# Kernel optimization log

Hardware: AMD Instinct MI355X
Metric: run time of the kernel (lower is better)

Reference implementation:

```python
import jax, jax.numpy as jnp
import numpy as np

B, H, T, N = 8, 12, 1024, 256  # N = mlp_internal_dim_multiplier * n_embd // n_head = 4*768//12
THETA = 2.0 ** 16


def _rope(phases, v):
    # interleaved rotate-half: pairs (even, odd) -> (-odd, even), as in torch stack+view
    v_rot = jnp.stack((-v[..., 1::2], v[..., ::2]), axis=-1).reshape(v.shape)
    ang = (phases % 1.0) * (2.0 * jnp.pi)
    return v * jnp.cos(ang) + v_rot * jnp.sin(ang)


def setup_inputs() -> dict:
    key = jax.random.key(0)
    k1, k2 = jax.random.split(key)
    Q = jax.random.normal(k1, (B, H, T, N), dtype=jnp.float32)
    V = jax.random.normal(k2, (B, H, T, N), dtype=jnp.float32)
    # frozen RoPE frequency buffer: pairs share a frequency, theta=2**16 (cycles/position)
    idx = (jnp.arange(N) // 2 * 2).astype(jnp.float32)
    freqs = (THETA ** (-idx / N)).reshape(1, 1, 1, N)
    return {"Q": Q, "V": V, "freqs": freqs}


def reference(Q, V, freqs):
    t = Q.shape[2]
    pos = jnp.arange(t, dtype=freqs.dtype).reshape(1, 1, -1, 1)
    phases = pos * freqs                      # [1,1,T,N]
    QR = _rope(phases, Q)                     # K is Q in Vision-BDH, so KR = QR
    scale = 1.0 / jnp.sqrt(jnp.asarray(Q.shape[-1], Q.dtype))
    scores = jnp.einsum("bhtn,bhsn->bhts", QR, QR) * scale  # [B,H,T,T]
    attn = jax.nn.softmax(scores, axis=-1)
    return jnp.einsum("bhts,bhsn->bhtn", attn, V)
```

## Files before the change

kernel.cpp:

```cpp
#include <hip/hip_runtime.h>
#include <stdint.h>

typedef __attribute__((ext_vector_type(8))) short short8;
typedef __attribute__((ext_vector_type(4))) float f32x4;
typedef __attribute__((ext_vector_type(16))) float f32x16;

#define BH 96
#define T 1024
#define D 256

static __device__ __forceinline__ unsigned short f2bf(float x){
  uint32_t u = __float_as_uint(x);
  uint32_t r = (u + 0x7FFFu + ((u >> 16) & 1u)) >> 16;
  return (unsigned short)r;
}

static __device__ __forceinline__ uint32_t cvtpk_bf16(float lo, float hi){
  uint32_t r;
  asm("v_cvt_pk_bf16_f32 %0, %1, %2" : "=v"(r) : "v"(lo), "v"(hi));
  return r;
}

static __device__ __forceinline__ float exp2_fast(float x){
  float r;
  asm("v_exp_f32 %0, %1" : "=v"(r) : "v"(x));
  return r;
}

static __device__ __forceinline__ void gload_lds16(const void* g, void* l){
  __builtin_amdgcn_global_load_lds((const __attribute__((address_space(1))) void*)g,
                                   (__attribute__((address_space(3))) void*)l, 16, 0, 0);
}

__global__ void k_rope(const float* __restrict__ Q, const float* __restrict__ freqs,
                       unsigned short* __restrict__ QR){
  const float SC = 0.25f * 1.20112241f;
  long idx = (long)blockIdx.x * 256 + threadIdx.x;
  long e = idx * 4;
  int n = (int)(e & (D - 1));
  int t = (int)((e >> 8) & (T - 1));
  float4 q = *(const float4*)(Q + e);
  float f0 = freqs[n];
  float f2 = freqs[n + 2];
  float ph0 = (float)t * f0; ph0 -= floorf(ph0);
  float ph2 = (float)t * f2; ph2 -= floorf(ph2);
  float c0 = __builtin_amdgcn_cosf(ph0), s0 = __builtin_amdgcn_sinf(ph0);
  float c2 = __builtin_amdgcn_cosf(ph2), s2 = __builtin_amdgcn_sinf(ph2);
  float o0 = (q.x * c0 - q.y * s0) * SC;
  float o1 = (q.y * c0 + q.x * s0) * SC;
  float o2 = (q.z * c2 - q.w * s2) * SC;
  float o3 = (q.w * c2 + q.z * s2) * SC;
  ushort4 o;
  o.x = f2bf(o0); o.y = f2bf(o1); o.z = f2bf(o2); o.w = f2bf(o3);
  *(ushort4*)(QR + e) = o;
}

__global__ void k_transpose(const float* __restrict__ V, unsigned short* __restrict__ Vt){
  __shared__ unsigned short L[64 * 66];
  int bid = blockIdx.x;
  int head = bid >> 6;
  int rem = bid & 63;
  int t0 = (rem & 15) * 64;
  int n0 = (rem >> 4) * 64;
  int tid = threadIdx.x;
  const float* Vh = V + (long)head * T * D;
  unsigned short* Vth = Vt + (long)head * T * D;
  int lr = tid >> 4;
  int lc = (tid & 15) * 4;
#pragma unroll
  for (int i = 0; i < 4; ++i){
    int tl = i * 16 + lr;
    float4 v = *(const float4*)(Vh + (long)(t0 + tl) * D + n0 + lc);
    uint32_t w0 = (uint32_t)f2bf(v.x) | ((uint32_t)f2bf(v.y) << 16);
    uint32_t w1 = (uint32_t)f2bf(v.z) | ((uint32_t)f2bf(v.w) << 16);
    *(uint32_t*)&L[tl * 66 + lc]     = w0;
    *(uint32_t*)&L[tl * 66 + lc + 2] = w1;
  }
  __syncthreads();
  int nr = tid >> 3;
  int t8 = (tid & 7) * 8;
#pragma unroll
  for (int i = 0; i < 2; ++i){
    int n_row = i * 32 + nr;
    unsigned short u[8];
#pragma unroll
    for (int j = 0; j < 8; ++j) u[j] = L[(t8 + j) * 66 + n_row];
    uint4 o;
    o.x = (uint32_t)u[0] | ((uint32_t)u[1] << 16);
    o.y = (uint32_t)u[2] | ((uint32_t)u[3] << 16);
    o.z = (uint32_t)u[4] | ((uint32_t)u[5] << 16);
    o.w = (uint32_t)u[6] | ((uint32_t)u[7] << 16);
    *(uint4*)(Vth + (long)(n0 + n_row) * T + t0 + t8) = o;
  }
}

__global__ __launch_bounds__(256, 2) void k_flash(const unsigned short* __restrict__ QR,
                                                  const unsigned short* __restrict__ Vt,
                                                  float* __restrict__ Out){
  __shared__ short lds[2][16384];
  int tid = threadIdx.x;
  int wid = tid >> 6, lane = tid & 63;
  int q31 = lane & 31, h = lane >> 5;

  int b = blockIdx.x;
  int xx = b & 7, sw = b >> 3;
  int qt = sw & 7, hg = sw >> 3;
  int head = hg * 8 + xx;

  const unsigned short* qr = QR + (long)head * T * D;
  const unsigned short* vt = Vt + (long)head * T * D;
  int qb = qt * 128 + wid * 32;

  int bK[4], bV[4];
#pragma unroll
  for (int j = 0; j < 4; ++j){
    int i = tid + j * 256;
    int c = i >> 6, s = i & 63;
    bK[j] = (s & 31) * 256 + (s >> 5) * 8 + c * 16;
    bV[j] = ((c >> 1) * 32 + (s & 31)) * 1024 + (c & 1) * 16 + (s >> 5) * 8;
  }

  short8 qf[16];
#pragma unroll
  for (int c = 0; c < 16; ++c)
    qf[c] = *(const short8*)(qr + (long)(qb + q31) * D + c * 16 + h * 8);

  const f32x16 Zv = {0.f,0.f,0.f,0.f,0.f,0.f,0.f,0.f,0.f,0.f,0.f,0.f,0.f,0.f,0.f,0.f};
  f32x16 acc[8];
#pragma unroll
  for (int i = 0; i < 8; ++i) acc[i] = Zv;
  float m = -3e38f, lsum = 0.f;

#pragma unroll
  for (int j = 0; j < 4; ++j){
    int i = tid + j * 256;
    gload_lds16(qr + bK[j], &lds[0][i * 8]);
    gload_lds16(vt + bV[j], &lds[0][8192 + i * 8]);
  }
  asm volatile("s_waitcnt vmcnt(0)" ::: "memory");
  __syncthreads();

  int buf = 0;
  for (int kb = 0; kb < T; kb += 32){
    if (kb + 32 < T){
      const unsigned short* sk = qr + (long)(kb + 32) * 256;
      const unsigned short* sv = vt + (kb + 32);
#pragma unroll
      for (int j = 0; j < 4; ++j){
        int i = tid + j * 256;
        gload_lds16(sk + bK[j], &lds[buf ^ 1][i * 8]);
        gload_lds16(sv + bV[j], &lds[buf ^ 1][8192 + i * 8]);
      }
    }
    const short* ldsK = &lds[buf][0];
    const short* ldsV = &lds[buf][8192];

    f32x16 sA = Zv, sB = Zv;
    __builtin_amdgcn_s_setprio(1);
#pragma unroll
    for (int c = 0; c < 8; ++c){
      short8 kf = *(const short8*)&ldsK[c * 512 + lane * 8];
      sA = __builtin_amdgcn_mfma_f32_32x32x16_bf16(kf, qf[c], sA, 0, 0, 0);
    }
#pragma unroll
    for (int c = 8; c < 16; ++c){
      short8 kf = *(const short8*)&ldsK[c * 512 + lane * 8];
      sB = __builtin_amdgcn_mfma_f32_32x32x16_bf16(kf, qf[c], sB, 0, 0, 0);
    }
    __builtin_amdgcn_s_setprio(0);
    f32x16 sc = sA + sB;

    float lm = fmaxf(fmaxf(fmaxf(sc[0], sc[1]), fmaxf(sc[2], sc[3])),
                     fmaxf(fmaxf(sc[4], sc[5]), fmaxf(sc[6], sc[7])));
    lm = fmaxf(lm, fmaxf(fmaxf(fmaxf(sc[8], sc[9]), fmaxf(sc[10], sc[11])),
                         fmaxf(fmaxf(sc[12], sc[13]), fmaxf(sc[14], sc[15]))));
    lm = fmaxf(lm, __shfl_xor(lm, 32));
    if (__any(lm > m + 11.0f)){
      float mn = fmaxf(m, lm);
      float a = exp2_fast(m - mn);
      m = mn;
      lsum *= a;
#pragma unroll
      for (int nb = 0; nb < 8; ++nb) acc[nb] *= a;
    }
    f32x16 p;
#pragma unroll
    for (int e = 0; e < 16; ++e) p[e] = exp2_fast(sc[e] - m);
    lsum += (((p[0]+p[1])+(p[2]+p[3])) + ((p[4]+p[5])+(p[6]+p[7])))
          + (((p[8]+p[9])+(p[10]+p[11])) + ((p[12]+p[13])+(p[14]+p[15])));

    uint32_t X0 = cvtpk_bf16(p[0],  p[1]);
    uint32_t X1 = cvtpk_bf16(p[2],  p[3]);
    uint32_t Y0 = cvtpk_bf16(p[4],  p[5]);
    uint32_t Y1 = cvtpk_bf16(p[6],  p[7]);
    uint32_t sX0 = __shfl_xor(X0, 32), sX1 = __shfl_xor(X1, 32);
    uint32_t sY0 = __shfl_xor(Y0, 32), sY1 = __shfl_xor(Y1, 32);
    uint4 f0;
    f0.x = h ? sY0 : X0;
    f0.y = h ? sY1 : X1;
    f0.z = h ? Y0  : sX0;
    f0.w = h ? Y1  : sX1;
    uint32_t Z0 = cvtpk_bf16(p[8],  p[9]);
    uint32_t Z1 = cvtpk_bf16(p[10], p[11]);
    uint32_t W0 = cvtpk_bf16(p[12], p[13]);
    uint32_t W1 = cvtpk_bf16(p[14], p[15]);
    uint32_t sZ0 = __shfl_xor(Z0, 32), sZ1 = __shfl_xor(Z1, 32);
    uint32_t sW0 = __shfl_xor(W0, 32), sW1 = __shfl_xor(W1, 32);
    uint4 f1;
    f1.x = h ? sW0 : Z0;
    f1.y = h ? sW1 : Z1;
    f1.z = h ? W0  : sZ0;
    f1.w = h ? W1  : sZ1;
    short8 pF0 = __builtin_bit_cast(short8, f0);
    short8 pF1 = __builtin_bit_cast(short8, f1);

    __builtin_amdgcn_s_setprio(1);
#pragma unroll
    for (int nb = 0; nb < 8; ++nb){
      short8 v0 = *(const short8*)&ldsV[(nb * 2 + 0) * 512 + lane * 8];
      short8 v1 = *(const short8*)&ldsV[(nb * 2 + 1) * 512 + lane * 8];
      acc[nb] = __builtin_amdgcn_mfma_f32_32x32x16_bf16(v0, pF0, acc[nb], 0, 0, 0);
      acc[nb] = __builtin_amdgcn_mfma_f32_32x32x16_bf16(v1, pF1, acc[nb], 0, 0, 0);
    }
    __builtin_amdgcn_s_setprio(0);

    asm volatile("s_waitcnt vmcnt(0)" ::: "memory");
    __syncthreads();
    buf ^= 1;
  }

  lsum += __shfl_xor(lsum, 32);
  float r = 1.0f / lsum;
  float* op = Out + (long)head * T * D + (long)(qb + q31) * D + h * 4;
#pragma unroll
  for (int nb = 0; nb < 8; ++nb){
#pragma unroll
    for (int rq = 0; rq < 4; ++rq){
      f32x4 o;
      o.x = acc[nb][rq * 4 + 0] * r;
      o.y = acc[nb][rq * 4 + 1] * r;
      o.z = acc[nb][rq * 4 + 2] * r;
      o.w = acc[nb][rq * 4 + 3] * r;
      *(f32x4*)(op + nb * 32 + rq * 8) = o;
    }
  }
}

extern "C" void kernel_launch(void* const* d_in, const int* in_sizes, int n_in,
                              void* d_out, int out_size, void* d_ws, size_t ws_size,
                              hipStream_t stream){
  (void)in_sizes; (void)n_in; (void)out_size; (void)ws_size;
  const float* Q     = (const float*)d_in[0];
  const float* V     = (const float*)d_in[1];
  const float* freqs = (const float*)d_in[2];
  float* Out = (float*)d_out;
  unsigned short* QR = (unsigned short*)d_ws;
  unsigned short* Vt = QR + (size_t)BH * T * D;
  k_rope<<<dim3((BH * T * D) / 4 / 256), dim3(256), 0, stream>>>(Q, freqs, QR);
  k_transpose<<<dim3(BH * 64), dim3(256), 0, stream>>>(V, Vt);
  k_flash<<<dim3(BH * 8), dim3(256), 0, stream>>>(QR, Vt, Out);
}
```

Measured before the change: 218.2 us.

## Make flash kernel persistent with triple-buffered LDS and partial vmcnt waits

```diff
diff --git a/kernel.cpp b/kernel.cpp
--- a/kernel.cpp
+++ b/kernel.cpp
@@ -84,7 +84,7 @@
     int n_row = i * 32 + nr;
     unsigned short u[8];
 #pragma unroll
-    for (int j = 0; j < 8; ++j) u[j] = L[(t8 + j) * 66 + n_row];
+    for (int jj = 0; jj < 8; ++jj) u[jj] = L[(t8 + jj) * 66 + n_row];
     uint4 o;
     o.x = (uint32_t)u[0] | ((uint32_t)u[1] << 16);
     o.y = (uint32_t)u[2] | ((uint32_t)u[3] << 16);
@@ -94,155 +94,163 @@
   }
 }
 
-__global__ __launch_bounds__(256, 2) void k_flash(const unsigned short* __restrict__ QR,
+__global__ __launch_bounds__(256, 1) void k_flash(const unsigned short* __restrict__ QR,
                                                   const unsigned short* __restrict__ Vt,
                                                   float* __restrict__ Out){
-  __shared__ short lds[2][16384];
+  __shared__ short lds[3][16384];
   int tid = threadIdx.x;
   int wid = tid >> 6, lane = tid & 63;
   int q31 = lane & 31, h = lane >> 5;
 
-  int b = blockIdx.x;
-  int xx = b & 7, sw = b >> 3;
-  int qt = sw & 7, hg = sw >> 3;
-  int head = hg * 8 + xx;
-
-  const unsigned short* qr = QR + (long)head * T * D;
-  const unsigned short* vt = Vt + (long)head * T * D;
-  int qb = qt * 128 + wid * 32;
+  int cu = blockIdx.x;
+  int x = cu & 7;
+  int jb = cu >> 3;
 
   int bK[4], bV[4];
 #pragma unroll
-  for (int j = 0; j < 4; ++j){
-    int i = tid + j * 256;
+  for (int jj = 0; jj < 4; ++jj){
+    int i = tid + jj * 256;
     int c = i >> 6, s = i & 63;
-    bK[j] = (s & 31) * 256 + (s >> 5) * 8 + c * 16;
-    bV[j] = ((c >> 1) * 32 + (s & 31)) * 1024 + (c & 1) * 16 + (s >> 5) * 8;
-  }
-
-  short8 qf[16];
-#pragma unroll
-  for (int c = 0; c < 16; ++c)
-    qf[c] = *(const short8*)(qr + (long)(qb + q31) * D + c * 16 + h * 8);
-
-  const f32x16 Zv = {0.f,0.f,0.f,0.f,0.f,0.f,0.f,0.f,0.f,0.f,0.f,0.f,0.f,0.f,0.f,0.f};
-  f32x16 acc[8];
-#pragma unroll
-  for (int i = 0; i < 8; ++i) acc[i] = Zv;
-  float m = -3e38f, lsum = 0.f;
-
-#pragma unroll
-  for (int j = 0; j < 4; ++j){
-    int i = tid + j * 256;
-    gload_lds16(qr + bK[j], &lds[0][i * 8]);
-    gload_lds16(vt + bV[j], &lds[0][8192 + i * 8]);
-  }
-  asm volatile("s_waitcnt vmcnt(0)" ::: "memory");
-  __syncthreads();
-
-  int buf = 0;
-  for (int kb = 0; kb < T; kb += 32){
-    if (kb + 32 < T){
-      const unsigned short* sk = qr + (long)(kb + 32) * 256;
-      const unsigned short* sv = vt + (kb + 32);
-#pragma unroll
-      for (int j = 0; j < 4; ++j){
-        int i = tid + j * 256;
-        gload_lds16(sk + bK[j], &lds[buf ^ 1][i * 8]);
-        gload_lds16(sv + bV[j], &lds[buf ^ 1][8192 + i * 8]);
-      }
+    bK[jj] = (s & 31) * 256 + (s >> 5) * 8 + c * 16;
+    bV[jj] = ((c >> 1) * 32 + (s & 31)) * 1024 + (c & 1) * 16 + (s >> 5) * 8;
+  }
+
+  for (int p = 0; p < 3; ++p){
+    int wl = jb + 32 * p;
+    int head = x * 12 + (wl >> 3);
+    int qt = wl & 7;
+    const unsigned short* qr = QR + (long)head * T * D;
+    const unsigned short* vt = Vt + (long)head * T * D;
+    int qb = qt * 128 + wid * 32;
+
+    auto stageT = [&](int slot, int tt){
+      const unsigned short* sk = qr + (long)tt * 8192;
+      const unsigned short* sv = vt + tt * 32;
+      short* kd = &lds[slot][0];
+      short* vd = &lds[slot][8192];
+#pragma unroll
+      for (int jj = 0; jj < 4; ++jj){
+        int i = tid + jj * 256;
+        gload_lds16(sk + bK[jj], kd + i * 8);
+        gload_lds16(sv + bV[jj], vd + i * 8);
+      }
+    };
+
+    short8 qf[16];
+#pragma unroll
+    for (int c = 0; c < 16; ++c)
+      qf[c] = *(const short8*)(qr + (long)(qb + q31) * D + c * 16 + h * 8);
+
+    const f32x16 Zv = {0.f,0.f,0.f,0.f,0.f,0.f,0.f,0.f,0.f,0.f,0.f,0.f,0.f,0.f,0.f,0.f};
+    f32x16 acc[8];
+#pragma unroll
+    for (int i = 0; i < 8; ++i) acc[i] = Zv;
+    float m = -3e38f, lsum = 0.f;
+
+    auto computeStep = [&](const short* ldsK, const short* ldsV){
+      f32x16 sA = Zv, sB = Zv;
+      __builtin_amdgcn_s_setprio(1);
+#pragma unroll
+      for (int c = 0; c < 8; ++c){
+        short8 kf = *(const short8*)&ldsK[c * 512 + lane * 8];
+        sA = __builtin_amdgcn_mfma_f32_32x32x16_bf16(kf, qf[c], sA, 0, 0, 0);
+      }
+#pragma unroll
+      for (int c = 8; c < 16; ++c){
+        short8 kf = *(const short8*)&ldsK[c * 512 + lane * 8];
+        sB = __builtin_amdgcn_mfma_f32_32x32x16_bf16(kf, qf[c], sB, 0, 0, 0);
+      }
+      __builtin_amdgcn_s_setprio(0);
+      f32x16 sc = sA + sB;
+
+      float lm = fmaxf(fmaxf(fmaxf(sc[0], sc[1]), fmaxf(sc[2], sc[3])),
+                       fmaxf(fmaxf(sc[4], sc[5]), fmaxf(sc[6], sc[7])));
+      lm = fmaxf(lm, fmaxf(fmaxf(fmaxf(sc[8], sc[9]), fmaxf(sc[10], sc[11])),
+                           fmaxf(fmaxf(sc[12], sc[13]), fmaxf(sc[14], sc[15]))));
+      lm = fmaxf(lm, __shfl_xor(lm, 32));
+      if (__any(lm > m + 11.0f)){
+        float mn = fmaxf(m, lm);
+        float a = exp2_fast(m - mn);
+        m = mn;
+        lsum *= a;
+#pragma unroll
+        for (int nb = 0; nb < 8; ++nb) acc[nb] *= a;
+      }
+      f32x16 pp;
+#pragma unroll
+      for (int e = 0; e < 16; ++e) pp[e] = exp2_fast(sc[e] - m);
+      lsum += (((pp[0]+pp[1])+(pp[2]+pp[3])) + ((pp[4]+pp[5])+(pp[6]+pp[7])))
+            + (((pp[8]+pp[9])+(pp[10]+pp[11])) + ((pp[12]+pp[13])+(pp[14]+pp[15])));
+
+      uint32_t X0 = cvtpk_bf16(pp[0],  pp[1]);
+      uint32_t X1 = cvtpk_bf16(pp[2],  pp[3]);
+      uint32_t Y0 = cvtpk_bf16(pp[4],  pp[5]);
+      uint32_t Y1 = cvtpk_bf16(pp[6],  pp[7]);
+      uint32_t sX0 = __shfl_xor(X0, 32), sX1 = __shfl_xor(X1, 32);
+      uint32_t sY0 = __shfl_xor(Y0, 32), sY1 = __shfl_xor(Y1, 32);
+      uint4 f0;
+      f0.x = h ? sY0 : X0;
+      f0.y = h ? sY1 : X1;
+      f0.z = h ? Y0  : sX0;
+      f0.w = h ? Y1  : sX1;
+      uint32_t Z0 = cvtpk_bf16(pp[8],  pp[9]);
+      uint32_t Z1 = cvtpk_bf16(pp[10], pp[11]);
+      uint32_t W0 = cvtpk_bf16(pp[12], pp[13]);
+      uint32_t W1 = cvtpk_bf16(pp[14], pp[15]);
+      uint32_t sZ0 = __shfl_xor(Z0, 32), sZ1 = __shfl_xor(Z1, 32);
+      uint32_t sW0 = __shfl_xor(W0, 32), sW1 = __shfl_xor(W1, 32);
+      uint4 f1;
+      f1.x = h ? sW0 : Z0;
+      f1.y = h ? sW1 : Z1;
+      f1.z = h ? W0  : sZ0;
+      f1.w = h ? W1  : sZ1;
+      short8 pF0 = __builtin_bit_cast(short8, f0);
+      short8 pF1 = __builtin_bit_cast(short8, f1);
+
+      __builtin_amdgcn_s_setprio(1);
+#pragma unroll
+      for (int nb = 0; nb < 8; ++nb){
+        short8 v0 = *(const short8*)&ldsV[(nb * 2 + 0) * 512 + lane * 8];
+        short8 v1 = *(const short8*)&ldsV[(nb * 2 + 1) * 512 + lane * 8];
+        acc[nb] = __builtin_amdgcn_mfma_f32_32x32x16_bf16(v0, pF0, acc[nb], 0, 0, 0);
+        acc[nb] = __builtin_amdgcn_mfma_f32_32x32x16_bf16(v1, pF1, acc[nb], 0, 0, 0);
+      }
+      __builtin_amdgcn_s_setprio(0);
+    };
+
+    stageT(0, 0);
+    stageT(1, 1);
+
+    int sl = 0, sp = 2;
+#pragma unroll 1
+    for (int t = 0; t < 31; ++t){
+      asm volatile("s_waitcnt vmcnt(8)" ::: "memory");
+      asm volatile("s_barrier" ::: "memory");
+      if (t + 2 < 32) stageT(sp, t + 2);
+      computeStep(&lds[sl][0], &lds[sl][8192]);
+      sl = (sl == 2) ? 0 : sl + 1;
+      sp = (sp == 2) ? 0 : sp + 1;
     }
-    const short* ldsK = &lds[buf][0];
-    const short* ldsV = &lds[buf][8192];
-
-    f32x16 sA = Zv, sB = Zv;
-    __builtin_amdgcn_s_setprio(1);
-#pragma unroll
-    for (int c = 0; c < 8; ++c){
-      short8 kf = *(const short8*)&ldsK[c * 512 + lane * 8];
-      sA = __builtin_amdgcn_mfma_f32_32x32x16_bf16(kf, qf[c], sA, 0, 0, 0);
+    asm volatile("s_waitcnt vmcnt(0)" ::: "memory");
+    asm volatile("s_barrier" ::: "memory");
+    computeStep(&lds[sl][0], &lds[sl][8192]);
+
+    lsum += __shfl_xor(lsum, 32);
+    float r = 1.0f / lsum;
+    float* op = Out + (long)head * T * D + (long)(qb + q31) * D + h * 4;
+#pragma unroll
+    for (int nb = 0; nb < 8; ++nb){
+#pragma unroll
+      for (int rq = 0; rq < 4; ++rq){
+        f32x4 o;
+        o.x = acc[nb][rq * 4 + 0] * r;
+        o.y = acc[nb][rq * 4 + 1] * r;
+        o.z = acc[nb][rq * 4 + 2] * r;
+        o.w = acc[nb][rq * 4 + 3] * r;
+        *(f32x4*)(op + nb * 32 + rq * 8) = o;
+      }
     }
-#pragma unroll
-    for (int c = 8; c < 16; ++c){
-      short8 kf = *(const short8*)&ldsK[c * 512 + lane * 8];
-      sB = __builtin_amdgcn_mfma_f32_32x32x16_bf16(kf, qf[c], sB, 0, 0, 0);
-    }
-    __builtin_amdgcn_s_setprio(0);
-    f32x16 sc = sA + sB;
-
-    float lm = fmaxf(fmaxf(fmaxf(sc[0], sc[1]), fmaxf(sc[2], sc[3])),
-                     fmaxf(fmaxf(sc[4], sc[5]), fmaxf(sc[6], sc[7])));
-    lm = fmaxf(lm, fmaxf(fmaxf(fmaxf(sc[8], sc[9]), fmaxf(sc[10], sc[11])),
-                         fmaxf(fmaxf(sc[12], sc[13]), fmaxf(sc[14], sc[15]))));
-    lm = fmaxf(lm, __shfl_xor(lm, 32));
-    if (__any(lm > m + 11.0f)){
-      float mn = fmaxf(m, lm);
-      float a = exp2_fast(m - mn);
-      m = mn;
-      lsum *= a;
-#pragma unroll
-      for (int nb = 0; nb < 8; ++nb) acc[nb] *= a;
-    }
-    f32x16 p;
-#pragma unroll
-    for (int e = 0; e < 16; ++e) p[e] = exp2_fast(sc[e] - m);
-    lsum += (((p[0]+p[1])+(p[2]+p[3])) + ((p[4]+p[5])+(p[6]+p[7])))
-          + (((p[8]+p[9])+(p[10]+p[11])) + ((p[12]+p[13])+(p[14]+p[15])));
-
-    uint32_t X0 = cvtpk_bf16(p[0],  p[1]);
-    uint32_t X1 = cvtpk_bf16(p[2],  p[3]);
-    uint32_t Y0 = cvtpk_bf16(p[4],  p[5]);
-    uint32_t Y1 = cvtpk_bf16(p[6],  p[7]);
-    uint32_t sX0 = __shfl_xor(X0, 32), sX1 = __shfl_xor(X1, 32);
-    uint32_t sY0 = __shfl_xor(Y0, 32), sY1 = __shfl_xor(Y1, 32);
-    uint4 f0;
-    f0.x = h ? sY0 : X0;
-    f0.y = h ? sY1 : X1;
-    f0.z = h ? Y0  : sX0;
-    f0.w = h ? Y1  : sX1;
-    uint32_t Z0 = cvtpk_bf16(p[8],  p[9]);
-    uint32_t Z1 = cvtpk_bf16(p[10], p[11]);
-    uint32_t W0 = cvtpk_bf16(p[12], p[13]);
-    uint32_t W1 = cvtpk_bf16(p[14], p[15]);
-    uint32_t sZ0 = __shfl_xor(Z0, 32), sZ1 = __shfl_xor(Z1, 32);
-    uint32_t sW0 = __shfl_xor(W0, 32), sW1 = __shfl_xor(W1, 32);
-    uint4 f1;
-    f1.x = h ? sW0 : Z0;
-    f1.y = h ? sW1 : Z1;
-    f1.z = h ? W0  : sZ0;
-    f1.w = h ? W1  : sZ1;
-    short8 pF0 = __builtin_bit_cast(short8, f0);
-    short8 pF1 = __builtin_bit_cast(short8, f1);
-
-    __builtin_amdgcn_s_setprio(1);
-#pragma unroll
-    for (int nb = 0; nb < 8; ++nb){
-      short8 v0 = *(const short8*)&ldsV[(nb * 2 + 0) * 512 + lane * 8];
-      short8 v1 = *(const short8*)&ldsV[(nb * 2 + 1) * 512 + lane * 8];
-      acc[nb] = __builtin_amdgcn_mfma_f32_32x32x16_bf16(v0, pF0, acc[nb], 0, 0, 0);
-      acc[nb] = __builtin_amdgcn_mfma_f32_32x32x16_bf16(v1, pF1, acc[nb], 0, 0, 0);
-    }
-    __builtin_amdgcn_s_setprio(0);
-
-    asm volatile("s_waitcnt vmcnt(0)" ::: "memory");
-    __syncthreads();
-    buf ^= 1;
-  }
-
-  lsum += __shfl_xor(lsum, 32);
-  float r = 1.0f / lsum;
-  float* op = Out + (long)head * T * D + (long)(qb + q31) * D + h * 4;
-#pragma unroll
-  for (int nb = 0; nb < 8; ++nb){
-#pragma unroll
-    for (int rq = 0; rq < 4; ++rq){
-      f32x4 o;
-      o.x = acc[nb][rq * 4 + 0] * r;
-      o.y = acc[nb][rq * 4 + 1] * r;
-      o.z = acc[nb][rq * 4 + 2] * r;
-      o.w = acc[nb][rq * 4 + 3] * r;
-      *(f32x4*)(op + nb * 32 + rq * 8) = o;
-    }
+    asm volatile("s_barrier" ::: "memory");
   }
 }
 
@@ -258,5 +266,5 @@
   unsigned short* Vt = QR + (size_t)BH * T * D;
   k_rope<<<dim3((BH * T * D) / 4 / 256), dim3(256), 0, stream>>>(Q, freqs, QR);
   k_transpose<<<dim3(BH * 64), dim3(256), 0, stream>>>(V, Vt);
-  k_flash<<<dim3(BH * 8), dim3(256), 0, stream>>>(QR, Vt, Out);
-}
+  k_flash<<<dim3(256), dim3(256), 0, stream>>>(QR, Vt, Out);
+}
```

Result: slower. 263.4 us (+20.7%).
